# Kernel tuning notes

Measured on AMD Instinct MI355X. Metric: run time of the kernel, lower is better.

The kernel has to match this reference:

```python
import jax, jax.numpy as jnp
import numpy as np

NUM_HEADS = 16
HIDDEN = 2048
HEAD_SIZE = HIDDEN // NUM_HEADS        # 128
ROTARY_PCT = 0.25
ROTARY_DIM = int(HEAD_SIZE * ROTARY_PCT)  # 32
ROTARY_BASE = 10000.0
BATCH = 4
SEQ = 1024
TOTAL = BATCH * SEQ


def setup_inputs() -> dict:
    key = jax.random.key(0)
    k1, k2, k3 = jax.random.split(key, 3)
    hidden_states = jax.random.normal(k1, (TOTAL, HIDDEN), dtype=jnp.float32)
    w_qkv = jax.random.normal(k2, (3 * HIDDEN, HIDDEN), dtype=jnp.float32) * (HIDDEN ** -0.5)
    b_qkv = jnp.zeros((3 * HIDDEN,), dtype=jnp.float32)
    w_dense = jax.random.normal(k3, (HIDDEN, HIDDEN), dtype=jnp.float32) * (HIDDEN ** -0.5)
    b_dense = jnp.zeros((HIDDEN,), dtype=jnp.float32)
    layer_past = jnp.zeros((TOTAL, 2, NUM_HEADS, HEAD_SIZE), dtype=jnp.float32)
    position_ids = jnp.tile(jnp.arange(SEQ, dtype=jnp.int64), BATCH)
    cu_seqlens = (jnp.arange(BATCH + 1, dtype=jnp.int32) * SEQ)
    return {
        "hidden_states": hidden_states, "layer_past": layer_past,
        "w_qkv": w_qkv, "b_qkv": b_qkv, "w_dense": w_dense, "b_dense": b_dense,
        "position_ids": position_ids, "cu_seqlens": cu_seqlens,
        "max_s": SEQ, "prefill": 1,
    }


def _apply_rotary(x, cos, sin):
    # x: [T, h, d]; GPT-NeoX (rotate-half, non-interleaved) on first ROTARY_DIM dims
    x_rot, x_pass = x[..., :ROTARY_DIM], x[..., ROTARY_DIM:]
    half = ROTARY_DIM // 2
    x1, x2 = x_rot[..., :half], x_rot[..., half:]
    return jnp.concatenate([x1 * cos - x2 * sin, x1 * sin + x2 * cos, x_pass], axis=-1)


def reference(hidden_states, layer_past, w_qkv, b_qkv, w_dense, b_dense,
              position_ids, cu_seqlens, max_s, prefill):
    # QKV projection: [T, 3H]
    qkv = hidden_states @ w_qkv.T + b_qkv
    # rearrange '... (h three d)' then permute -> [T, 3, h, d]
    qkv = qkv.reshape(TOTAL, NUM_HEADS, 3, HEAD_SIZE).transpose(0, 2, 1, 3)

    # rotary cos/sin per token position: [T, 1, ROTARY_DIM/2]
    inv_freq = 1.0 / (ROTARY_BASE ** (jnp.arange(0, ROTARY_DIM, 2, dtype=jnp.float32) / ROTARY_DIM))
    freqs = position_ids.astype(jnp.float32)[:, None] * inv_freq[None, :]
    cos = jnp.cos(freqs)[:, None, :]
    sin = jnp.sin(freqs)[:, None, :]

    q = _apply_rotary(qkv[:, 0], cos, sin)   # [T, h, d]
    k = _apply_rotary(qkv[:, 1], cos, sin)
    v = qkv[:, 2]

    # prefill: cache write layer_past[...] = kv_rot (byproduct, not returned here)
    # ragged causal flash attention; all sequences have equal length SEQ here
    qb = q.reshape(BATCH, SEQ, NUM_HEADS, HEAD_SIZE)
    kb = k.reshape(BATCH, SEQ, NUM_HEADS, HEAD_SIZE)
    vb = v.reshape(BATCH, SEQ, NUM_HEADS, HEAD_SIZE)

    scale = HEAD_SIZE ** -0.5
    scores = jnp.einsum('bqhd,bkhd->bhqk', qb, kb) * scale  # [B, h, S, S]
    causal = jnp.tril(jnp.ones((SEQ, SEQ), dtype=bool))
    scores = jnp.where(causal[None, None], scores, jnp.finfo(scores.dtype).min)
    probs = jax.nn.softmax(scores, axis=-1)
    attn = jnp.einsum('bhqk,bkhd->bqhd', probs, vb)          # [B, S, h, d]
    attn = attn.reshape(TOTAL, HIDDEN)

    return attn @ w_dense.T + b_dense
```

## Files before the change

kernel.cpp:

```cpp
#include <hip/hip_runtime.h>
#include <stdint.h>

#define NUM_HEADS 16
#define HIDDEN    2048
#define HEAD_SIZE 128
#define TOTAL     4096
#define SEQ       1024
#define QKV_N     (3*HIDDEN)

typedef __bf16 bf16x8 __attribute__((ext_vector_type(8)));
typedef float  f32x4  __attribute__((ext_vector_type(4)));

__device__ __forceinline__ unsigned short f2bf(float f) {
  unsigned u = __float_as_uint(f);
  u += 0x7FFFu + ((u >> 16) & 1u);
  return (unsigned short)(u >> 16);
}
__device__ __forceinline__ float bf2f(unsigned short h) {
  return __uint_as_float(((unsigned)h) << 16);
}
__device__ __forceinline__ void cp16(void* lds, const void* g) {
  __builtin_amdgcn_global_load_lds(
      (const __attribute__((address_space(1))) void*)g,
      (__attribute__((address_space(3))) void*)lds, 16, 0, 0);
}

__global__ __launch_bounds__(256) void f32_to_bf16_multi(
    const float* __restrict__ a, unsigned short* __restrict__ oa, int na,
    const float* __restrict__ b, unsigned short* __restrict__ ob, int nb,
    const float* __restrict__ c, unsigned short* __restrict__ oc, int nc)
{
  int i = (blockIdx.x * 256 + threadIdx.x) * 4;
  const float* src; unsigned short* dst;
  if (i < na)            { src = a; dst = oa; }
  else if (i < na + nb)  { i -= na; src = b; dst = ob; }
  else                   { i -= na + nb; if (i >= nc) return; src = c; dst = oc; }
  float4 v = *(const float4*)(src + i);
  unsigned p0 = (unsigned)f2bf(v.x) | ((unsigned)f2bf(v.y) << 16);
  unsigned p1 = (unsigned)f2bf(v.z) | ((unsigned)f2bf(v.w) << 16);
  uint2 pk; pk.x = p0; pk.y = p1;
  *(uint2*)(dst + i) = pk;
}

#define SBAR()   __builtin_amdgcn_sched_barrier(0)
#define HBAR()   __builtin_amdgcn_s_barrier()
#define WLGKM0() asm volatile("s_waitcnt lgkmcnt(0)" ::: "memory")
#define WVMC(n)  asm volatile("s_waitcnt vmcnt(" #n ")" ::: "memory")
#define PH_SYNC() do { SBAR(); HBAR(); WLGKM0(); SBAR(); } while (0)
#define PH_END()  do { SBAR(); HBAR(); } while (0)

__device__ __forceinline__ void stage2(char* lb, const char* sb, int o0, int o1,
                                       size_t gg0, size_t gg1) {
  cp16(lb + o0, sb + gg0);
  cp16(lb + o1, sb + gg1);
}

template<int MH>
__device__ __forceinline__ void ldA4(bf16x8 (&d)[4][2], const unsigned short* ls,
                                     int base, int ch0) {
#pragma unroll
  for (int mi = 0; mi < 4; mi++) {
    d[mi][0] = *(const bf16x8*)((const char*)ls + base + (MH*4 + mi)*2048 + ch0);
    d[mi][1] = *(const bf16x8*)((const char*)ls + base + (MH*4 + mi)*2048 + (ch0 ^ 64));
  }
}
template<int NH>
__device__ __forceinline__ void ldB2(bf16x8 (&d)[2][2], const unsigned short* ls,
                                     int base, int ch0) {
#pragma unroll
  for (int ni = 0; ni < 2; ni++) {
    d[ni][0] = *(const bf16x8*)((const char*)ls + base + (NH*2 + ni)*2048 + ch0);
    d[ni][1] = *(const bf16x8*)((const char*)ls + base + (NH*2 + ni)*2048 + (ch0 ^ 64));
  }
}
template<int MH, int NH>
__device__ __forceinline__ void mfmaQ(f32x4 (&acc)[8][4], const bf16x8 (&AF)[4][2],
                                      const bf16x8 (&BF)[2][2]) {
  __builtin_amdgcn_s_setprio(1);
#pragma unroll
  for (int kk = 0; kk < 2; kk++)
#pragma unroll
    for (int mi = 0; mi < 4; mi++)
#pragma unroll
      for (int ni = 0; ni < 2; ni++)
        acc[MH*4 + mi][NH*2 + ni] = __builtin_amdgcn_mfma_f32_16x16x32_bf16(
            AF[mi][kk], BF[ni][kk], acc[MH*4 + mi][NH*2 + ni], 0, 0, 0);
  __builtin_amdgcn_s_setprio(0);
}

__global__ __launch_bounds__(512, 2) void gemm_qkv_8ph(
    const unsigned short* __restrict__ A,
    const unsigned short* __restrict__ B,
    const float* __restrict__ bias,
    const int* __restrict__ pos_ids,
    unsigned short* __restrict__ Qb,
    unsigned short* __restrict__ Kb,
    unsigned short* __restrict__ Vt)
{
  __shared__ unsigned short lsA[2][256*64];
  __shared__ unsigned short lsB[2][256*64];

  const int tid  = threadIdx.x;
  const int w    = tid >> 6, lane = tid & 63;
  const int quad = lane >> 4, lm = lane & 15;
  const int wm   = w >> 2, wn = w & 3;

  const int g  = ((int)blockIdx.x & 7) * 48 + ((int)blockIdx.x >> 3);
  const int my = g & 15, nx = g >> 4;
  const int mBase = my * 256, nBase = nx * 256;

  const int off0 = tid * 16;
  const int off1 = off0 + 8192;
  const int r0 = off0 >> 7, r1 = off1 >> 7;
  const size_t g0 = (size_t)r0 * (HIDDEN*2) + ((((off0 >> 4) & 7) ^ (r0 & 7)) << 4);
  const size_t g1 = (size_t)r1 * (HIDDEN*2) + ((((off1 >> 4) & 7) ^ (r1 & 7)) << 4);
  const char* Abase = (const char*)A + (size_t)mBase * HIDDEN * 2;
  const char* Bbase = (const char*)B + (size_t)nBase * HIDDEN * 2;

  const int ch0   = ((quad ^ (lm & 7)) << 4);
  const int aBase = (wm * 128 + lm) * 128;
  const int bBase = (wn * 64  + lm) * 128;

#define STG(bi, h, t) stage2( \
    (((h) < 2) ? (char*)&lsA[bi][0] : (char*)&lsB[bi][0]) + (((h) & 1) * 16384), \
    (((h) < 2) ? Abase : Bbase) + (size_t)((h) & 1) * (128 * HIDDEN * 2) + (size_t)(t) * 128, \
    off0, off1, g0, g1)

  const f32x4 zero4 = {0.f, 0.f, 0.f, 0.f};
  f32x4 acc[8][4];
#pragma unroll
  for (int i = 0; i < 8; i++)
#pragma unroll
    for (int j = 0; j < 4; j++) acc[i][j] = zero4;

  bf16x8 a0[4][2], a1[4][2], b0[2][2], b1[2][2];

  STG(0, 0, 0); STG(0, 1, 0); STG(0, 2, 0); STG(0, 3, 0);
  STG(1, 0, 1); STG(1, 1, 1);
  WVMC(4);
  SBAR(); HBAR();

#pragma unroll 1
  for (int t = 0; t < 30; t += 2) {
    ldA4<0>(a0, &lsA[0][0], aBase, ch0);
    ldB2<0>(b0, &lsB[0][0], bBase, ch0);
    STG(1, 2, t + 1);
    PH_SYNC(); mfmaQ<0,0>(acc, a0, b0); PH_END();

    ldA4<1>(a1, &lsA[0][0], aBase, ch0);
    STG(1, 3, t + 1);
    PH_SYNC(); mfmaQ<1,0>(acc, a1, b0); PH_END();

    ldB2<1>(b1, &lsB[0][0], bBase, ch0);
    STG(0, 0, t + 2);
    PH_SYNC(); mfmaQ<0,1>(acc, a0, b1); PH_END();

    STG(0, 1, t + 2);
    WVMC(4);
    PH_SYNC(); mfmaQ<1,1>(acc, a1, b1); PH_END();

    ldA4<0>(a0, &lsA[1][0], aBase, ch0);
    ldB2<0>(b0, &lsB[1][0], bBase, ch0);
    STG(0, 2, t + 2);
    PH_SYNC(); mfmaQ<0,0>(acc, a0, b0); PH_END();

    ldA4<1>(a1, &lsA[1][0], aBase, ch0);
    STG(0, 3, t + 2);
    PH_SYNC(); mfmaQ<1,0>(acc, a1, b0); PH_END();

    ldB2<1>(b1, &lsB[1][0], bBase, ch0);
    STG(1, 0, t + 3);
    PH_SYNC(); mfmaQ<0,1>(acc, a0, b1); PH_END();

    STG(1, 1, t + 3);
    WVMC(4);
    PH_SYNC(); mfmaQ<1,1>(acc, a1, b1); PH_END();
  }

  ldA4<0>(a0, &lsA[0][0], aBase, ch0);
  ldB2<0>(b0, &lsB[0][0], bBase, ch0);
  STG(1, 2, 31);
  PH_SYNC(); mfmaQ<0,0>(acc, a0, b0); PH_END();

  ldA4<1>(a1, &lsA[0][0], aBase, ch0);
  STG(1, 3, 31);
  PH_SYNC(); mfmaQ<1,0>(acc, a1, b0); PH_END();

  ldB2<1>(b1, &lsB[0][0], bBase, ch0);
  PH_SYNC(); mfmaQ<0,1>(acc, a0, b1); PH_END();

  WVMC(0);
  PH_SYNC(); mfmaQ<1,1>(acc, a1, b1); PH_END();

  ldA4<0>(a0, &lsA[1][0], aBase, ch0);
  ldB2<0>(b0, &lsB[1][0], bBase, ch0);
  PH_SYNC(); mfmaQ<0,0>(acc, a0, b0); PH_END();

  ldA4<1>(a1, &lsA[1][0], aBase, ch0);
  PH_SYNC(); mfmaQ<1,0>(acc, a1, b0); PH_END();

  ldB2<1>(b1, &lsB[1][0], bBase, ch0);
  PH_SYNC(); mfmaQ<0,1>(acc, a0, b1); PH_END();

  PH_SYNC(); mfmaQ<1,1>(acc, a1, b1);
#undef STG

  const int col0  = nBase + wn * 64;
  const int chunk = col0 >> 7;
  const int hh = chunk / 3, tq = chunk - 3 * hh;
  const int dbase = col0 & 127;

  if (tq == 2) {
#pragma unroll
    for (int nf = 0; nf < 4; nf++) {
      int d = dbase + nf * 16 + lm;
      float bv = bias[col0 + nf * 16 + lm];
#pragma unroll
      for (int mf = 0; mf < 8; mf++) {
        int row0 = mBase + wm * 128 + mf * 16 + quad * 4;
        int b = row0 >> 10, s0 = row0 & 1023;
        unsigned u0 = (unsigned)f2bf(acc[mf][nf][0] + bv) | ((unsigned)f2bf(acc[mf][nf][1] + bv) << 16);
        unsigned u1 = (unsigned)f2bf(acc[mf][nf][2] + bv) | ((unsigned)f2bf(acc[mf][nf][3] + bv) << 16);
        uint2 pk; pk.x = u0; pk.y = u1;
        *(uint2*)(Vt + ((size_t)(b * NUM_HEADS + hh) * HEAD_SIZE + d) * SEQ + s0) = pk;
      }
    }
  } else {
    unsigned short* dst = (tq == 0) ? Qb : Kb;
    if (dbase == 0) {
      const float inv = exp2f(-0.8304820237f * (float)lm);
      const float bv0 = bias[col0 + lm];
      const float bv1 = bias[col0 + 16 + lm];
#pragma unroll
      for (int mf = 0; mf < 8; mf++) {
        int row0 = mBase + wm * 128 + mf * 16 + quad * 4;
#pragma unroll
        for (int r = 0; r < 4; r++) {
          int row = row0 + r;
          int b = row >> 10, s = row & 1023;
          float pos = (float)pos_ids[row];
          float sn, cs;
          sincosf(pos * inv, &sn, &cs);
          float x1 = acc[mf][0][r] + bv0;
          float x2 = acc[mf][1][r] + bv1;
          size_t rb = ((size_t)(b * NUM_HEADS + hh) * SEQ + s) * HEAD_SIZE;
          dst[rb + lm]      = f2bf(x1 * cs - x2 * sn);
          dst[rb + 16 + lm] = f2bf(x1 * sn + x2 * cs);
        }
      }
#pragma unroll
      for (int nf = 2; nf < 4; nf++) {
        int d = nf * 16 + lm;
        float bv = bias[col0 + d];
#pragma unroll
        for (int mf = 0; mf < 8; mf++) {
          int row0 = mBase + wm * 128 + mf * 16 + quad * 4;
#pragma unroll
          for (int r = 0; r < 4; r++) {
            int row = row0 + r;
            int b = row >> 10, s = row & 1023;
            dst[((size_t)(b * NUM_HEADS + hh) * SEQ + s) * HEAD_SIZE + d] = f2bf(acc[mf][nf][r] + bv);
          }
        }
      }
    } else {
#pragma unroll
      for (int nf = 0; nf < 4; nf++) {
        int d = 64 + nf * 16 + lm;
        float bv = bias[col0 + nf * 16 + lm];
#pragma unroll
        for (int mf = 0; mf < 8; mf++) {
          int row0 = mBase + wm * 128 + mf * 16 + quad * 4;
#pragma unroll
          for (int r = 0; r < 4; r++) {
            int row = row0 + r;
            int b = row >> 10, s = row & 1023;
            dst[((size_t)(b * NUM_HEADS + hh) * SEQ + s) * HEAD_SIZE + d] = f2bf(acc[mf][nf][r] + bv);
          }
        }
      }
    }
  }
}

__global__ __launch_bounds__(256) void gemm_dense(
    const unsigned short* __restrict__ A,
    const unsigned short* __restrict__ B,
    const float* __restrict__ bias,
    float* __restrict__ Cf,
    int M, int N, int K)
{
  __shared__ unsigned short lsA[2][128*32];
  __shared__ unsigned short lsB[2][128*32];
  const int tid  = threadIdx.x;
  const int w    = tid >> 6, lane = tid & 63;
  const int quad = lane >> 4, lm = lane & 15;
  const int wm   = w & 1, wn = w >> 1;
  const int mBase = blockIdx.y * 128;
  const int nBase = blockIdx.x * 128;
  const int swz = (lm >> 1) & 3;

  const f32x4 zero4 = {0.f, 0.f, 0.f, 0.f};
  f32x4 acc[4][4];
#pragma unroll
  for (int i = 0; i < 4; i++)
#pragma unroll
    for (int j = 0; j < 4; j++) acc[i][j] = zero4;

  const int cg = ((tid & 3) ^ ((tid >> 3) & 3)) * 16;

  auto stage = [&](int bufi, int k0) {
#pragma unroll
    for (int i = 0; i < 2; i++) {
      int off = i * 4096 + tid * 16;
      int row = off >> 6;
      cp16((char*)&lsA[bufi][0] + off, (const char*)(A + (size_t)(mBase + row) * K + k0) + cg);
    }
#pragma unroll
    for (int i = 0; i < 2; i++) {
      int off = i * 4096 + tid * 16;
      int row = off >> 6;
      cp16((char*)&lsB[bufi][0] + off, (const char*)(B + (size_t)(nBase + row) * K + k0) + cg);
    }
  };

  int buf = 0;
  stage(0, 0);

  for (int k0 = 0; k0 < K; k0 += 32) {
    __syncthreads();
    bf16x8 af[4], bfr[4];
#pragma unroll
    for (int mf = 0; mf < 4; mf++)
      af[mf] = *(const bf16x8*)(&lsA[buf][(wm * 64 + mf * 16 + lm) * 32 + (quad ^ swz) * 8]);
#pragma unroll
    for (int nf = 0; nf < 4; nf++)
      bfr[nf] = *(const bf16x8*)(&lsB[buf][(wn * 64 + nf * 16 + lm) * 32 + (quad ^ swz) * 8]);
    if (k0 + 32 < K) stage(buf ^ 1, k0 + 32);
#pragma unroll
    for (int mf = 0; mf < 4; mf++)
#pragma unroll
      for (int nf = 0; nf < 4; nf++)
        acc[mf][nf] = __builtin_amdgcn_mfma_f32_16x16x32_bf16(af[mf], bfr[nf], acc[mf][nf], 0, 0, 0);
    buf ^= 1;
  }

#pragma unroll
  for (int nf = 0; nf < 4; nf++) {
    int col = nBase + wn * 64 + nf * 16 + lm;
    float bv = bias[col];
#pragma unroll
    for (int mf = 0; mf < 4; mf++) {
      int row0 = mBase + wm * 64 + mf * 16 + quad * 4;
#pragma unroll
      for (int r = 0; r < 4; r++)
        Cf[(size_t)(row0 + r) * N + col] = acc[mf][nf][r] + bv;
    }
  }
}

__global__ __launch_bounds__(256, 2) void flash_attn_k(
    const unsigned short* __restrict__ Q,
    const unsigned short* __restrict__ K,
    const unsigned short* __restrict__ VT,
    unsigned short* __restrict__ O)
{
  const int bh = blockIdx.x;
  const int pair = blockIdx.y;
  const int qa = 15 - pair, qb = pair;
  const int b = bh >> 4, h = bh & 15;
  const size_t base = (size_t)bh * SEQ * HEAD_SIZE;
  const unsigned short* Qp = Q + base;
  const unsigned short* Kp = K + base;
  const unsigned short* Vp = VT + base;

  __shared__ unsigned short Ks[2][4][64*32];
  __shared__ unsigned short Vl[2][128*64];
  __shared__ unsigned short Ps[64][72];

  const int tid  = threadIdx.x;
  const int w    = tid >> 6, lane = tid & 63;
  const int quad = lane >> 4, lm = lane & 15;
  const int swz4 = (lm >> 1) & 3;
  const int swz8 = lm & 7;
  const int cgK = ((tid & 3) ^ ((tid >> 3) & 3)) * 8;
  const int cgV = ((tid & 7) ^ ((tid >> 3) & 7)) * 8;

  const float K1 = 0.1275156876f;
  const f32x4 zero4 = {0.f, 0.f, 0.f, 0.f};
  const __bf16 one = (__bf16)1.0f;
  const bf16x8 vones = {one, one, one, one, one, one, one, one};

  auto stage = [&](int buf, int kt) {
    const unsigned short* krow = Kp + (size_t)(kt * 64 + (tid >> 2)) * HEAD_SIZE + cgK;
#pragma unroll
    for (int kk = 0; kk < 4; kk++)
      cp16((char*)&Ks[buf][kk][0] + tid * 16, krow + kk * 32);
#pragma unroll
    for (int i = 0; i < 4; i++) {
      int off = i * 4096 + tid * 16;
      int d = off >> 7;
      cp16((char*)&Vl[buf][0] + off, Vp + (size_t)d * SEQ + kt * 64 + cgV);
    }
  };

  int buf = 0;
  stage(0, 0);

  for (int ph = 0; ph < 2; ph++) {
    const int qt = ph ? qb : qa;
    bf16x8 qf[4];
    {
      const unsigned short* qrow = Qp + (size_t)(qt * 64 + w * 16 + lm) * HEAD_SIZE;
#pragma unroll
      for (int kk = 0; kk < 4; kk++)
        qf[kk] = *(const bf16x8*)(qrow + kk * 32 + quad * 8);
    }
    float m_r[4];
#pragma unroll
    for (int r = 0; r < 4; r++) m_r[r] = -1e30f;
    f32x4 lacc = zero4;
    f32x4 o[8];
#pragma unroll
    for (int i = 0; i < 8; i++) o[i] = zero4;

    for (int kt = 0; kt <= qt; ++kt) {
      __syncthreads();
      bool last = (ph == 1) && (kt == qt);
      if (!last) stage(buf ^ 1, (kt < qt) ? kt + 1 : 0);

      f32x4 sf[4];
#pragma unroll
      for (int nf = 0; nf < 4; nf++) {
        f32x4 accs = zero4;
#pragma unroll
        for (int kk = 0; kk < 4; kk++) {
          bf16x8 kfrag = *(const bf16x8*)(&Ks[buf][kk][(nf * 16 + lm) * 32 + (quad ^ swz4) * 8]);
          accs = __builtin_amdgcn_mfma_f32_16x16x32_bf16(qf[kk], kfrag, accs, 0, 0, 0);
        }
        sf[nf] = accs;
      }
      if (kt == qt) {
        int qrow0 = qt * 64 + w * 16 + quad * 4;
#pragma unroll
        for (int nf = 0; nf < 4; nf++) {
          int col = kt * 64 + nf * 16 + lm;
#pragma unroll
          for (int r = 0; r < 4; r++)
            if (col > qrow0 + r) sf[nf][r] = -1e30f;
        }
      }
      float alpha[4];
#pragma unroll
      for (int r = 0; r < 4; r++) {
        float v = fmaxf(fmaxf(sf[0][r], sf[1][r]), fmaxf(sf[2][r], sf[3][r]));
        v = fmaxf(v, __shfl_xor(v, 1));
        v = fmaxf(v, __shfl_xor(v, 2));
        v = fmaxf(v, __shfl_xor(v, 4));
        v = fmaxf(v, __shfl_xor(v, 8));
        float mn = fmaxf(m_r[r], v);
        alpha[r] = exp2f((m_r[r] - mn) * K1);
        m_r[r] = mn;
      }
#pragma unroll
      for (int nf = 0; nf < 4; nf++)
#pragma unroll
        for (int r = 0; r < 4; r++) {
          float p = exp2f((sf[nf][r] - m_r[r]) * K1);
          Ps[w * 16 + quad * 4 + r][nf * 16 + lm] = f2bf(p);
        }
#pragma unroll
      for (int df = 0; df < 8; df++)
#pragma unroll
        for (int r = 0; r < 4; r++) o[df][r] *= alpha[r];
#pragma unroll
      for (int r = 0; r < 4; r++) lacc[r] *= alpha[r];

#pragma unroll
      for (int ks = 0; ks < 2; ks++) {
        bf16x8 pf = *(const bf16x8*)(&Ps[w * 16 + lm][ks * 32 + quad * 8]);
        lacc = __builtin_amdgcn_mfma_f32_16x16x32_bf16(pf, vones, lacc, 0, 0, 0);
#pragma unroll
        for (int df = 0; df < 8; df++) {
          bf16x8 vf = *(const bf16x8*)(&Vl[buf][(df * 16 + lm) * 64 + (((ks * 4 + quad) ^ swz8)) * 8]);
          o[df] = __builtin_amdgcn_mfma_f32_16x16x32_bf16(pf, vf, o[df], 0, 0, 0);
        }
      }
      buf ^= 1;
    }

    float rl[4];
#pragma unroll
    for (int r = 0; r < 4; r++) rl[r] = 1.f / lacc[r];
    int row0 = b * SEQ + qt * 64 + w * 16 + quad * 4;
#pragma unroll
    for (int df = 0; df < 8; df++) {
      int col = h * HEAD_SIZE + df * 16 + lm;
#pragma unroll
      for (int r = 0; r < 4; r++)
        O[(size_t)(row0 + r) * HIDDEN + col] = f2bf(o[df][r] * rl[r]);
    }
  }
}

extern "C" void kernel_launch(void* const* d_in, const int* in_sizes, int n_in,
                              void* d_out, int out_size, void* d_ws, size_t ws_size,
                              hipStream_t stream)
{
  const float* hs   = (const float*)d_in[0];
  const float* wqkv = (const float*)d_in[2];
  const float* bqkv = (const float*)d_in[3];
  const float* wd   = (const float*)d_in[4];
  const float* bd   = (const float*)d_in[5];
  const int*   pos  = (const int*)d_in[6];

  char* ws = (char*)d_ws;
  unsigned short* hsb = (unsigned short*)ws;  ws += (size_t)TOTAL * HIDDEN * 2;
  unsigned short* wqb = (unsigned short*)ws;  ws += (size_t)QKV_N * HIDDEN * 2;
  unsigned short* wdb = (unsigned short*)ws;  ws += (size_t)HIDDEN * HIDDEN * 2;
  unsigned short* Qb  = (unsigned short*)ws;  ws += (size_t)TOTAL * HIDDEN * 2;
  unsigned short* Kb  = (unsigned short*)ws;  ws += (size_t)TOTAL * HIDDEN * 2;
  unsigned short* Vt  = (unsigned short*)ws;  ws += (size_t)TOTAL * HIDDEN * 2;
  unsigned short* attnb = hsb;
  if (ws_size < (size_t)(ws - (char*)d_ws)) return;

  const int na = TOTAL * HIDDEN, nb = QKV_N * HIDDEN, nc = HIDDEN * HIDDEN;
  f32_to_bf16_multi<<<(na + nb + nc) / 1024, 256, 0, stream>>>(
      hs, hsb, na, wqkv, wqb, nb, wd, wdb, nc);

  gemm_qkv_8ph<<<dim3(384), 512, 0, stream>>>(hsb, wqb, bqkv, pos, Qb, Kb, Vt);

  flash_attn_k<<<dim3(64, 8), 256, 0, stream>>>(Qb, Kb, Vt, attnb);

  gemm_dense<<<dim3(HIDDEN / 128, TOTAL / 128), 256, 0, stream>>>(
      attnb, wdb, bd, (float*)d_out, TOTAL, HIDDEN, HIDDEN);
}
```

Before: 398.6 us.

## Prefetch LDS fragments one phase ahead with partial lgkmcnt waits in QKV GEMM

Restructures the QKV GEMM main loop into a software pipeline. LDS reads for the next MFMA quadrant are issued before the current quadrant's MFMAs, and the full lgkmcnt(0) wait becomes partial waits (lgkmcnt 12/8/4/0), so LDS latency overlaps matrix work. The global-to-LDS wait thresholds shift from vmcnt(4) to vmcnt(2) to fit the new ordering. The risk is correctness if any partial wait count is off, since the counts depend on exactly how many LDS instructions the compiler emits.

```diff
diff --git a/kernel.cpp b/kernel.cpp
--- a/kernel.cpp
+++ b/kernel.cpp
@@ -44,9 +44,9 @@
 
 #define SBAR()   __builtin_amdgcn_sched_barrier(0)
 #define HBAR()   __builtin_amdgcn_s_barrier()
-#define WLGKM0() asm volatile("s_waitcnt lgkmcnt(0)" ::: "memory")
 #define WVMC(n)  asm volatile("s_waitcnt vmcnt(" #n ")" ::: "memory")
-#define PH_SYNC() do { SBAR(); HBAR(); WLGKM0(); SBAR(); } while (0)
+#define PH_PRE(n) do { SBAR(); HBAR(); \
+    asm volatile("s_waitcnt lgkmcnt(" #n ")" ::: "memory"); SBAR(); } while (0)
 #define PH_END()  do { SBAR(); HBAR(); } while (0)
 
 __device__ __forceinline__ void stage2(char* lb, const char* sb, int o0, int o1,
@@ -139,70 +139,70 @@
   STG(1, 0, 1); STG(1, 1, 1);
   WVMC(4);
   SBAR(); HBAR();
+  ldA4<0>(a0, &lsA[0][0], aBase, ch0);
+  ldB2<0>(b0, &lsB[0][0], bBase, ch0);
 
 #pragma unroll 1
   for (int t = 0; t < 30; t += 2) {
+    ldA4<1>(a1, &lsA[0][0], aBase, ch0);
+    STG(1, 2, t + 1);
+    PH_PRE(8); mfmaQ<0,0>(acc, a0, b0); PH_END();
+
+    ldB2<1>(b1, &lsB[0][0], bBase, ch0);
+    STG(1, 3, t + 1);
+    PH_PRE(4); mfmaQ<1,0>(acc, a1, b0); PH_END();
+
+    STG(0, 0, t + 2);
+    WVMC(2);
+    PH_PRE(0); mfmaQ<0,1>(acc, a0, b1); PH_END();
+
+    ldA4<0>(a0, &lsA[1][0], aBase, ch0);
+    ldB2<0>(b0, &lsB[1][0], bBase, ch0);
+    STG(0, 1, t + 2);
+    PH_PRE(12); mfmaQ<1,1>(acc, a1, b1); PH_END();
+
+    ldA4<1>(a1, &lsA[1][0], aBase, ch0);
+    STG(0, 2, t + 2);
+    PH_PRE(8); mfmaQ<0,0>(acc, a0, b0); PH_END();
+
+    ldB2<1>(b1, &lsB[1][0], bBase, ch0);
+    STG(0, 3, t + 2);
+    PH_PRE(4); mfmaQ<1,0>(acc, a1, b0); PH_END();
+
+    STG(1, 0, t + 3);
+    WVMC(2);
+    PH_PRE(0); mfmaQ<0,1>(acc, a0, b1); PH_END();
+
     ldA4<0>(a0, &lsA[0][0], aBase, ch0);
     ldB2<0>(b0, &lsB[0][0], bBase, ch0);
-    STG(1, 2, t + 1);
-    PH_SYNC(); mfmaQ<0,0>(acc, a0, b0); PH_END();
-
-    ldA4<1>(a1, &lsA[0][0], aBase, ch0);
-    STG(1, 3, t + 1);
-    PH_SYNC(); mfmaQ<1,0>(acc, a1, b0); PH_END();
-
-    ldB2<1>(b1, &lsB[0][0], bBase, ch0);
-    STG(0, 0, t + 2);
-    PH_SYNC(); mfmaQ<0,1>(acc, a0, b1); PH_END();
-
-    STG(0, 1, t + 2);
-    WVMC(4);
-    PH_SYNC(); mfmaQ<1,1>(acc, a1, b1); PH_END();
-
-    ldA4<0>(a0, &lsA[1][0], aBase, ch0);
-    ldB2<0>(b0, &lsB[1][0], bBase, ch0);
-    STG(0, 2, t + 2);
-    PH_SYNC(); mfmaQ<0,0>(acc, a0, b0); PH_END();
-
-    ldA4<1>(a1, &lsA[1][0], aBase, ch0);
-    STG(0, 3, t + 2);
-    PH_SYNC(); mfmaQ<1,0>(acc, a1, b0); PH_END();
-
-    ldB2<1>(b1, &lsB[1][0], bBase, ch0);
-    STG(1, 0, t + 3);
-    PH_SYNC(); mfmaQ<0,1>(acc, a0, b1); PH_END();
-
     STG(1, 1, t + 3);
-    WVMC(4);
-    PH_SYNC(); mfmaQ<1,1>(acc, a1, b1); PH_END();
-  }
-
-  ldA4<0>(a0, &lsA[0][0], aBase, ch0);
-  ldB2<0>(b0, &lsB[0][0], bBase, ch0);
+    PH_PRE(12); mfmaQ<1,1>(acc, a1, b1); PH_END();
+  }
+
+  ldA4<1>(a1, &lsA[0][0], aBase, ch0);
   STG(1, 2, 31);
-  PH_SYNC(); mfmaQ<0,0>(acc, a0, b0); PH_END();
-
-  ldA4<1>(a1, &lsA[0][0], aBase, ch0);
+  PH_PRE(8); mfmaQ<0,0>(acc, a0, b0); PH_END();
+
+  ldB2<1>(b1, &lsB[0][0], bBase, ch0);
   STG(1, 3, 31);
-  PH_SYNC(); mfmaQ<1,0>(acc, a1, b0); PH_END();
-
-  ldB2<1>(b1, &lsB[0][0], bBase, ch0);
-  PH_SYNC(); mfmaQ<0,1>(acc, a0, b1); PH_END();
+  PH_PRE(4); mfmaQ<1,0>(acc, a1, b0); PH_END();
 
   WVMC(0);
-  PH_SYNC(); mfmaQ<1,1>(acc, a1, b1); PH_END();
+  PH_PRE(0); mfmaQ<0,1>(acc, a0, b1); PH_END();
 
   ldA4<0>(a0, &lsA[1][0], aBase, ch0);
   ldB2<0>(b0, &lsB[1][0], bBase, ch0);
-  PH_SYNC(); mfmaQ<0,0>(acc, a0, b0); PH_END();
+  PH_PRE(12); mfmaQ<1,1>(acc, a1, b1); PH_END();
 
   ldA4<1>(a1, &lsA[1][0], aBase, ch0);
-  PH_SYNC(); mfmaQ<1,0>(acc, a1, b0); PH_END();
+  PH_PRE(8); mfmaQ<0,0>(acc, a0, b0); PH_END();
 
   ldB2<1>(b1, &lsB[1][0], bBase, ch0);
-  PH_SYNC(); mfmaQ<0,1>(acc, a0, b1); PH_END();
-
-  PH_SYNC(); mfmaQ<1,1>(acc, a1, b1);
+  PH_PRE(4); mfmaQ<1,0>(acc, a1, b0); PH_END();
+
+  PH_PRE(0); mfmaQ<0,1>(acc, a0, b1); PH_END();
+
+  PH_PRE(0); mfmaQ<1,1>(acc, a1, b1);
 #undef STG
 
   const int col0  = nBase + wn * 64;
```

After: 425.8 us. +6.8%, slower.
